# Performance work log

Measured on AMD Instinct MI355X. Metric: run time of the kernel, lower is better.

The kernel has to match this reference:

```python
import jax, jax.numpy as jnp
import numpy as np

B, T, I, H, O = 1024, 16384, 1, 1, 1


def setup_inputs() -> dict:
    key = jax.random.key(0)
    ks = jax.random.split(key, 7)
    return {
        "x":    jax.random.normal(ks[0], (B, T, I), dtype=jnp.float32),
        # torch LSTM params, gate order (i, f, g, o)
        "w_ih": jax.random.normal(ks[1], (4 * H, I), dtype=jnp.float32) * 0.5,
        "w_hh": jax.random.normal(ks[2], (4 * H, H), dtype=jnp.float32) * 0.5,
        "b_ih": jax.random.normal(ks[3], (4 * H,), dtype=jnp.float32) * 0.1,
        "b_hh": jax.random.normal(ks[4], (4 * H,), dtype=jnp.float32) * 0.1,
        # trailing Linear(hidden_size -> output_size)
        "W":    jax.random.normal(ks[5], (O, H), dtype=jnp.float32) * 0.5,
        "b":    jax.random.normal(ks[6], (O,), dtype=jnp.float32) * 0.1,
    }


def reference(x, w_ih, w_hh, b_ih, b_hh, W, b):
    # Single-layer batch_first LSTM (zero initial state), then pointwise Linear.
    Bb, Tt, _ = x.shape
    Hh = w_hh.shape[1]
    # Precompute input contribution for all timesteps: [B, T, 4H]
    xg = jnp.einsum('bti,gi->btg', x, w_ih) + b_ih + b_hh
    xg = jnp.swapaxes(xg, 0, 1)  # [T, B, 4H] for scan over time

    def step(carry, xt):
        h, c = carry
        gates = xt + h @ w_hh.T  # [B, 4H]
        i, f, g, o = jnp.split(gates, 4, axis=-1)
        i = jax.nn.sigmoid(i)
        f = jax.nn.sigmoid(f)
        g = jnp.tanh(g)
        o = jax.nn.sigmoid(o)
        c = f * c + i * g
        h = o * jnp.tanh(c)
        return (h, c), h

    h0 = jnp.zeros((Bb, Hh), dtype=x.dtype)
    c0 = jnp.zeros((Bb, Hh), dtype=x.dtype)
    _, ys = jax.lax.scan(step, (h0, c0), xg)  # ys: [T, B, H]
    y = jnp.swapaxes(ys, 0, 1)                # [B, T, H]
    # Linear applied pointwise over the hidden dim (the torch view/reshape is a no-op math-wise)
    return y @ W.T + b                        # [B, T, O]
```

## Files before the change

### kernel.cpp

```cpp
#include <hip/hip_runtime.h>
#include <stdint.h>

#define T_LEN  16384
#define B_N    1024
#define CHUNKS 256
#define CL     (T_LEN / CHUNKS)
#define WARM   32

#define LOG2E  1.4426950408889634f

typedef __attribute__((address_space(3))) uint32_t lds_u32;
typedef __attribute__((address_space(1))) const uint32_t glb_u32;

__device__ __forceinline__ void dma16(const float* g, float* l)
{
    __builtin_amdgcn_global_load_lds((glb_u32*)g, (lds_u32*)l, 16, 0, 0);
}


__global__ __launch_bounds__(256) void lstm_chunk_kernel(
    const float* __restrict__ x,
    const float* __restrict__ w_ih,
    const float* __restrict__ w_hh,
    const float* __restrict__ b_ih,
    const float* __restrict__ b_hh,
    const float* __restrict__ Wlin,
    const float* __restrict__ blin,
    float* __restrict__ y)
{
    __shared__ float sbuf[2][4][1024];

    const int tid = threadIdx.x;
    const int w   = tid >> 6;
    const int l   = tid & 63;
    const int gid = blockIdx.x * 256 + tid;
    const int j   = gid >> 10;
    const int b   = gid & (B_N - 1);
    const int bw  = b & ~63;

    const float ki = -LOG2E, kt = 2.0f * LOG2E;
    const float wi = w_ih[0] * ki, wf = w_ih[1] * ki, wg = w_ih[2] * kt, wo = w_ih[3] * ki;
    const float ui = w_hh[0] * ki, uf = w_hh[1] * ki, ug = w_hh[2] * kt, uo = w_hh[3] * ki;
    const float bi = (b_ih[0] + b_hh[0]) * ki;
    const float bf = (b_ih[1] + b_hh[1]) * ki;
    const float bg = (b_ih[2] + b_hh[2]) * kt;
    const float bo = (b_ih[3] + b_hh[3]) * ki;
    const float Wy = Wlin[0], by = blin[0];

    const int start  = j * CL;
    const int warm   = j ? WARM : 0;
    const int wstart = start - warm;
    const int nblk   = (CL + warm) >> 4;
    const int nwarm  = warm >> 4;

    const int rq  = l >> 2;
    const int rsw = rq & 3;
    const int qsw = (l >> 4) & 3;
    const int gL  = (l & 3) ^ qsw;
    const int sSt = (l & 3) ^ rsw;
    const int gSt = sSt ^ qsw;

    uint32_t xoff[4], yoff[4];
    #pragma unroll
    for (int q = 0; q < 4; ++q) {
        const uint32_t r = (uint32_t)(bw + 16 * q + rq);
        xoff[q] = r * T_LEN + (uint32_t)wstart + 4u * (uint32_t)gL;
        yoff[q] = r * T_LEN + (uint32_t)start  + 4u * (uint32_t)gSt;
    }

    float* bufA = &sbuf[0][w][0];
    float* bufB = &sbuf[1][w][0];

    #pragma unroll
    for (int q = 0; q < 4; ++q) dma16(x + xoff[q], bufA + 256 * q);
    asm volatile("s_waitcnt vmcnt(0)" ::: "memory");

    float cur[16] __attribute__((aligned(16)));
    #pragma unroll
    for (int g = 0; g < 4; ++g)
        *(float4*)(cur + 4 * g) = *(const float4*)(bufA + 16 * l + 4 * (g ^ rsw));

    float h = 0.0f, c = 0.0f;

    for (int blk = 0; blk < nblk; ++blk) {
        const bool more = (blk + 1 < nblk);

        if (more) {
            #pragma unroll
            for (int q = 0; q < 4; ++q)
                dma16(x + xoff[q] + ((blk + 1) << 4), bufB + 256 * q);
            asm volatile("" ::: "memory");
        }

        float yv[16] __attribute__((aligned(16)));
        #pragma unroll
        for (int k = 0; k < 16; ++k) {
            const float xv = cur[k];
            const float pi = fmaf(h, ui, fmaf(xv, wi, bi));
            const float pf = fmaf(h, uf, fmaf(xv, wf, bf));
            const float pg = fmaf(h, ug, fmaf(xv, wg, bg));
            const float po = fmaf(h, uo, fmaf(xv, wo, bo));
            const float ei = __builtin_amdgcn_exp2f(pi);
            const float ef = __builtin_amdgcn_exp2f(pf);
            const float eg = __builtin_amdgcn_exp2f(pg);
            const float eo = __builtin_amdgcn_exp2f(po);
            const float ai  = 1.0f + ei;
            const float af  = 1.0f + ef;
            const float ag  = 1.0f + eg;
            const float aig = ai * ag;
            const float n_c = fmaf(c, aig, (eg - 1.0f) * af);
            c = n_c * __builtin_amdgcn_rcpf(af * aig);
            const float ct = fminf(kt * c, 126.0f);
            const float et = __builtin_amdgcn_exp2f(ct);
            h = (et - 1.0f) * __builtin_amdgcn_rcpf((1.0f + eo) * (1.0f + et));
            yv[k] = fmaf(h, Wy, by);
        }

        if (blk >= nwarm) {
            #pragma unroll
            for (int g = 0; g < 4; ++g)
                *(float4*)(bufA + 16 * l + 4 * (g ^ rsw)) = *(const float4*)(yv + 4 * g);
            const int ob = (blk - nwarm) << 4;
            #pragma unroll
            for (int q = 0; q < 4; ++q) {
                const float4 sv = *(const float4*)(bufA + 256 * q + 16 * rq + 4 * sSt);
                *(float4*)(y + yoff[q] + ob) = sv;
            }
        }

        if (more) {
            if (blk >= nwarm) asm volatile("s_waitcnt vmcnt(4)" ::: "memory");
            else              asm volatile("s_waitcnt vmcnt(0)" ::: "memory");
            #pragma unroll
            for (int g = 0; g < 4; ++g)
                *(float4*)(cur + 4 * g) = *(const float4*)(bufB + 16 * l + 4 * (g ^ rsw));
            float* t = bufA; bufA = bufB; bufB = t;
        }
    }
}

extern "C" void kernel_launch(void* const* d_in, const int* in_sizes, int n_in,
                              void* d_out, int out_size, void* d_ws, size_t ws_size,
                              hipStream_t stream) {
    const float* x    = (const float*)d_in[0];
    const float* w_ih = (const float*)d_in[1];
    const float* w_hh = (const float*)d_in[2];
    const float* b_ih = (const float*)d_in[3];
    const float* b_hh = (const float*)d_in[4];
    const float* Wlin = (const float*)d_in[5];
    const float* blin = (const float*)d_in[6];
    float* y = (float*)d_out;

    const int total_threads = B_N * CHUNKS;
    lstm_chunk_kernel<<<dim3(total_threads / 256), dim3(256), 0, stream>>>(
        x, w_ih, w_hh, b_ih, b_hh, Wlin, blin, y);
}
```

Measured before the change: 140.6 us.

## Double chunk count, single-buffer LDS, and store outputs directly from registers

Doubles the number of time chunks so each thread walks a shorter serial sequence and more threads run in parallel, and adds an occupancy hint to launch_bounds. The LDS double buffer becomes a single buffer: the current block is copied into registers before the next DMA is issued into the same buffer. Outputs are now written as four float4 stores per thread straight from registers instead of being transposed through LDS for coalescing. Shorter chunks make the fixed 32-step warm-up a larger share of the work, and the uncoalesced strided stores may waste memory bandwidth.

```diff
diff --git a/kernel.cpp b/kernel.cpp
--- a/kernel.cpp
+++ b/kernel.cpp
@@ -3,7 +3,7 @@
 
 #define T_LEN  16384
 #define B_N    1024
-#define CHUNKS 256
+#define CHUNKS 512
 #define CL     (T_LEN / CHUNKS)
 #define WARM   32
 
@@ -18,7 +18,7 @@
 }
 
 
-__global__ __launch_bounds__(256) void lstm_chunk_kernel(
+__global__ __launch_bounds__(256, 8) void lstm_chunk_kernel(
     const float* __restrict__ x,
     const float* __restrict__ w_ih,
     const float* __restrict__ w_hh,
@@ -28,7 +28,7 @@
     const float* __restrict__ blin,
     float* __restrict__ y)
 {
-    __shared__ float sbuf[2][4][1024];
+    __shared__ float sbuf[4][1024];
 
     const int tid = threadIdx.x;
     const int w   = tid >> 6;
@@ -57,38 +57,37 @@
     const int rsw = rq & 3;
     const int qsw = (l >> 4) & 3;
     const int gL  = (l & 3) ^ qsw;
-    const int sSt = (l & 3) ^ rsw;
-    const int gSt = sSt ^ qsw;
 
-    uint32_t xoff[4], yoff[4];
+    uint32_t xoff[4];
     #pragma unroll
     for (int q = 0; q < 4; ++q) {
         const uint32_t r = (uint32_t)(bw + 16 * q + rq);
         xoff[q] = r * T_LEN + (uint32_t)wstart + 4u * (uint32_t)gL;
-        yoff[q] = r * T_LEN + (uint32_t)start  + 4u * (uint32_t)gSt;
     }
 
-    float* bufA = &sbuf[0][w][0];
-    float* bufB = &sbuf[1][w][0];
+    float* buf = &sbuf[w][0];
+    float* yp  = y + (size_t)b * T_LEN + start;
 
     #pragma unroll
-    for (int q = 0; q < 4; ++q) dma16(x + xoff[q], bufA + 256 * q);
-    asm volatile("s_waitcnt vmcnt(0)" ::: "memory");
-
-    float cur[16] __attribute__((aligned(16)));
-    #pragma unroll
-    for (int g = 0; g < 4; ++g)
-        *(float4*)(cur + 4 * g) = *(const float4*)(bufA + 16 * l + 4 * (g ^ rsw));
+    for (int q = 0; q < 4; ++q) dma16(x + xoff[q], buf + 256 * q);
 
     float h = 0.0f, c = 0.0f;
 
     for (int blk = 0; blk < nblk; ++blk) {
-        const bool more = (blk + 1 < nblk);
+        if (blk <= nwarm) asm volatile("s_waitcnt vmcnt(0)" ::: "memory");
+        else              asm volatile("s_waitcnt vmcnt(4)" ::: "memory");
 
-        if (more) {
+        float cur[16] __attribute__((aligned(16)));
+        #pragma unroll
+        for (int g = 0; g < 4; ++g)
+            *(float4*)(cur + 4 * g) = *(const float4*)(buf + 16 * l + 4 * (g ^ rsw));
+
+        asm volatile("s_waitcnt lgkmcnt(0)" ::: "memory");
+
+        if (blk + 1 < nblk) {
             #pragma unroll
             for (int q = 0; q < 4; ++q)
-                dma16(x + xoff[q] + ((blk + 1) << 4), bufB + 256 * q);
+                dma16(x + xoff[q] + ((blk + 1) << 4), buf + 256 * q);
             asm volatile("" ::: "memory");
         }
 
@@ -117,24 +116,11 @@
         }
 
         if (blk >= nwarm) {
-            #pragma unroll
-            for (int g = 0; g < 4; ++g)
-                *(float4*)(bufA + 16 * l + 4 * (g ^ rsw)) = *(const float4*)(yv + 4 * g);
-            const int ob = (blk - nwarm) << 4;
-            #pragma unroll
-            for (int q = 0; q < 4; ++q) {
-                const float4 sv = *(const float4*)(bufA + 256 * q + 16 * rq + 4 * sSt);
-                *(float4*)(y + yoff[q] + ob) = sv;
-            }
-        }
-
-        if (more) {
-            if (blk >= nwarm) asm volatile("s_waitcnt vmcnt(4)" ::: "memory");
-            else              asm volatile("s_waitcnt vmcnt(0)" ::: "memory");
-            #pragma unroll
-            for (int g = 0; g < 4; ++g)
-                *(float4*)(cur + 4 * g) = *(const float4*)(bufB + 16 * l + 4 * (g ^ rsw));
-            float* t = bufA; bufA = bufB; bufB = t;
+            float4* yo = (float4*)(yp + ((blk - nwarm) << 4));
+            yo[0] = *(float4*)(yv + 0);
+            yo[1] = *(float4*)(yv + 4);
+            yo[2] = *(float4*)(yv + 8);
+            yo[3] = *(float4*)(yv + 12);
         }
     }
 }
```

Measured after the change: 158.5 us. 1.13x slower.
